# Performance work log

Measured on AMD Instinct MI355X. Metric: run time of the kernel, lower is better.

## Reference

```python
import jax, jax.numpy as jnp
import numpy as np

B, N, VF, EF, DV, DE, LN = 64, 64, 32, 16, 128, 128, 4
EPS_INNER = 128.0  # BatchNorm1d(MAX_N, internal_d_vert): 2nd positional arg is eps (faithful to source bug)
EPS_BN = 1e-5


def gev_layer(v_in, e_in, evW, evb, eW, eb, vW, vb, relu=True):
    act = jax.nn.relu if relu else (lambda x: x)
    ev = v_in @ evW + evb                                   # [B,N,De]
    # outer_v_sum: ev.unsqueeze(1) + ev.unsqueeze(2) -> [B,N,N,De]
    e_out = act(e_in @ eW + eb + ev[:, None, :, :] + ev[:, :, None, :])
    per_v_e = e_out.sum(axis=1)                             # sum-aggregate over dim 1
    v_out = act(jnp.concatenate([per_v_e, v_in], axis=-1) @ vW + vb)
    return v_out, e_out


def bn_flat(v, g, b):
    # BatchNorm1d(N*VF) on [B, N*VF] in training mode (biased var)
    x = v.reshape(-1, N * VF)
    mu = x.mean(axis=0)
    var = x.var(axis=0)
    x = (x - mu) * jax.lax.rsqrt(var + EPS_BN) * g + b
    return x.reshape(-1, N, VF)


def bn_inner(v, g, b):
    # BatchNorm1d(MAX_N, eps=128) on [B, N, D]: channels are the N axis, stats over (B, D)
    mu = v.mean(axis=(0, 2), keepdims=True)
    var = v.var(axis=(0, 2), keepdims=True)
    return (v - mu) * jax.lax.rsqrt(var + EPS_INNER) * g[None, :, None] + b[None, :, None]


def setup_inputs() -> dict:
    key = jax.random.key(0)
    ks = jax.random.split(key, 24)
    s = 0.01  # force_lin_init with init_noise=0.01, biases zero
    nrm = lambda k, shp: jax.random.normal(k, shp, dtype=jnp.float32) * s
    inp = {
        "v": jax.random.normal(ks[0], (B, N, VF), dtype=jnp.float32),
        "e": jax.random.normal(ks[1], (B, N, N, EF), dtype=jnp.float32),
        "bn_in_g": jnp.ones((N * VF,), jnp.float32),
        "bn_in_b": jnp.zeros((N * VF,), jnp.float32),
        "g1_evW": nrm(ks[2], (VF, DE)), "g1_evb": jnp.zeros((DE,), jnp.float32),
        "g1_eW": nrm(ks[3], (EF, DE)), "g1_eb": jnp.zeros((DE,), jnp.float32),
        "g1_vW": nrm(ks[4], (VF + DE, DV)), "g1_vb": jnp.zeros((DV,), jnp.float32),
        "inn_evW": nrm(ks[5], (LN, DV, DE)), "inn_evb": jnp.zeros((LN, DE), jnp.float32),
        "inn_eW": nrm(ks[6], (LN, DE, DE)), "inn_eb": jnp.zeros((LN, DE), jnp.float32),
        "inn_vW": nrm(ks[7], (LN, DV + DE, DV)), "inn_vb": jnp.zeros((LN, DV), jnp.float32),
        "bn_g": jnp.ones((LN, N), jnp.float32),
        "bn_b": jnp.zeros((LN, N), jnp.float32),
        "g3_evW": nrm(ks[8], (DV, 1)), "g3_evb": jnp.zeros((1,), jnp.float32),
        "g3_eW": nrm(ks[9], (DE, 1)), "g3_eb": jnp.zeros((1,), jnp.float32),
        "g3_vW": nrm(ks[10], (DV + 1, 1)), "g3_vb": jnp.zeros((1,), jnp.float32),
    }
    return inp


def reference(v, e, bn_in_g, bn_in_b, g1_evW, g1_evb, g1_eW, g1_eb, g1_vW, g1_vb,
              inn_evW, inn_evb, inn_eW, inn_eb, inn_vW, inn_vb, bn_g, bn_b,
              g3_evW, g3_evb, g3_eW, g3_eb, g3_vW, g3_vb):
    v = bn_flat(v, bn_in_g, bn_in_b)
    v, e = gev_layer(v, e, g1_evW, g1_evb, g1_eW, g1_eb, g1_vW, g1_vb)
    for i in range(LN):
        v_next, e_next = gev_layer(v, e, inn_evW[i], inn_evb[i], inn_eW[i], inn_eb[i], inn_vW[i], inn_vb[i])
        v = v_next + v  # resnet
        e = e_next + e
        v = bn_inner(v, bn_g[i], bn_b[i])
    v, e = gev_layer(v, e, g3_evW, g3_evb, g3_eW, g3_eb, g3_vW, g3_vb, relu=False)
    return v, e
```

## Files before the change

### kernel.cpp

```cpp
#include <hip/hip_runtime.h>
#include <hip/hip_bf16.h>


typedef __bf16 bf16_t;
typedef __bf16 bf16x8 __attribute__((ext_vector_type(8)));
typedef __bf16 bf16x4 __attribute__((ext_vector_type(4)));
typedef float f32x4 __attribute__((ext_vector_type(4)));

__device__ __forceinline__ void bar_lgkm() {
  asm volatile("s_waitcnt lgkmcnt(0)\n\ts_barrier" ::: "memory");
}

__global__ __launch_bounds__(256) void k_prep(const float* __restrict__ vin,
    const float* __restrict__ g, const float* __restrict__ bt,
    const float* __restrict__ eW, float* __restrict__ v0,
    bf16_t* __restrict__ Wt, float* __restrict__ stats) {
  const int blk = blockIdx.x, tid = threadIdx.x;
  if (blk < 8) {
    int ch = blk * 256 + tid;
    float s = 0.f, s2 = 0.f;
    for (int b = 0; b < 64; ++b) { float x = vin[b * 2048 + ch]; s += x; s2 += x * x; }
    float mu = s * (1.f / 64.f);
    float var = s2 * (1.f / 64.f) - mu * mu;
    float sc = rsqrtf(var + 1e-5f) * g[ch];
    float bb = bt[ch];
    for (int b = 0; b < 64; ++b) {
      float x = vin[b * 2048 + ch];
      v0[b * 2048 + ch] = (x - mu) * sc + bb;
    }
  } else if (blk < 264) {
    int idx = (blk - 8) * 256 + tid;
    int l = idx >> 14, r = idx & 16383, n = r >> 7, k = r & 127;
    Wt[idx] = (bf16_t)eW[(l << 14) + (k << 7) + n];
  } else {
    for (int i = tid; i < 512; i += 256) stats[i] = 0.f;
  }
}

template <int K>
__global__ __launch_bounds__(128) void k_ev(const float* __restrict__ v_in,
    const float* __restrict__ W, const float* __restrict__ bias,
    float* __restrict__ out) {
  __shared__ float rows[8][K];
  const int r0 = blockIdx.x * 8;
  const int c = threadIdx.x;
  for (int idx = c; idx < 8 * K; idx += 128) {
    int rr = idx / K, kk = idx % K;
    rows[rr][kk] = v_in[(r0 + rr) * K + kk];
  }
  __syncthreads();
  float acc[8];
  const float bv = bias[c];
#pragma unroll
  for (int r = 0; r < 8; ++r) acc[r] = bv;
  for (int k4 = 0; k4 < K; k4 += 4) {
    float w0 = W[(k4 + 0) * 128 + c], w1 = W[(k4 + 1) * 128 + c];
    float w2 = W[(k4 + 2) * 128 + c], w3 = W[(k4 + 3) * 128 + c];
#pragma unroll
    for (int r = 0; r < 8; ++r) {
      float4 x = *(const float4*)&rows[r][k4];
      acc[r] += x.x * w0 + x.y * w1 + x.z * w2 + x.w * w3;
    }
  }
#pragma unroll
  for (int r = 0; r < 8; ++r) out[(r0 + r) * 128 + c] = acc[r];
}

__global__ __launch_bounds__(128) void k_evbn(float* __restrict__ v,
    const float* __restrict__ stats, const float* __restrict__ g,
    const float* __restrict__ bt, const float* __restrict__ W,
    const float* __restrict__ bias, float* __restrict__ out) {
  __shared__ float rows[8][128];
  const int r0 = blockIdx.x * 8;
  const int c = threadIdx.x;
#pragma unroll
  for (int rr = 0; rr < 8; ++rr) {
    int n = (r0 + rr) & 63;
    float mu = stats[n] * (1.f / 8192.f);
    float var = stats[64 + n] * (1.f / 8192.f) - mu * mu;
    float sc = rsqrtf(var + 128.f) * g[n];
    float x = (v[(r0 + rr) * 128 + c] - mu) * sc + bt[n];
    rows[rr][c] = x;
    v[(r0 + rr) * 128 + c] = x;
  }
  __syncthreads();
  float acc[8];
  const float bv = bias[c];
#pragma unroll
  for (int r = 0; r < 8; ++r) acc[r] = bv;
  for (int k4 = 0; k4 < 128; k4 += 4) {
    float w0 = W[(k4 + 0) * 128 + c], w1 = W[(k4 + 1) * 128 + c];
    float w2 = W[(k4 + 2) * 128 + c], w3 = W[(k4 + 3) * 128 + c];
#pragma unroll
    for (int r = 0; r < 8; ++r) {
      float4 x = *(const float4*)&rows[r][k4];
      acc[r] += x.x * w0 + x.y * w1 + x.z * w2 + x.w * w3;
    }
  }
#pragma unroll
  for (int r = 0; r < 8; ++r) out[(r0 + r) * 128 + c] = acc[r];
}

__global__ __launch_bounds__(256) void k_edge_g1(const float* __restrict__ e0,
    const float* __restrict__ eW, const float* __restrict__ eb,
    const float* __restrict__ ev, bf16_t* __restrict__ e_ws,
    float* __restrict__ pve) {
  __shared__ bf16_t A0s[2][64][40];
  __shared__ bf16_t Os[2][64][136];
  const int b = blockIdx.x >> 5, j0 = (blockIdx.x & 31) * 2;
  const int tid = threadIdx.x;
  const int lane = tid & 63, w = tid >> 6;
  const int quad = lane >> 4, l16 = lane & 15;
#pragma unroll
  for (int t = 0; t < 2; ++t) {
    int idx = tid + t * 256;
    int row = idx >> 3, off = (idx & 7) * 4;
    int jc = off >> 4, k = off & 15;
    f32x4 x = *(const f32x4*)&e0[((b * 64 + row) * 64 + j0) * 16 + off];
    bf16x4 y;
#pragma unroll
    for (int r = 0; r < 4; ++r) y[r] = (bf16_t)x[r];
    *(bf16x4*)&A0s[jc][row][k] = y;
    bf16x4 z = {(bf16_t)0.f, (bf16_t)0.f, (bf16_t)0.f, (bf16_t)0.f};
    *(bf16x4*)&A0s[jc][row][16 + k] = z;
  }
  const int c0[2] = {w * 32 + quad * 4, w * 32 + 16 + quad * 4};
  bf16x8 wf[2];
#pragma unroll
  for (int nt = 0; nt < 2; ++nt) {
    const int c = w * 32 + nt * 16 + l16;
#pragma unroll
    for (int jj = 0; jj < 8; ++jj)
      wf[nt][jj] = (quad < 2) ? (bf16_t)eW[(quad * 8 + jj) * 128 + c] : (bf16_t)0.f;
  }
  f32x4 acc[2][4][2];
  {
    f32x4 ebv[2], evj[2][2], evi[4][2];
#pragma unroll
    for (int nt = 0; nt < 2; ++nt) {
      ebv[nt] = *(const f32x4*)&eb[c0[nt]];
#pragma unroll
      for (int jc = 0; jc < 2; ++jc)
        evj[jc][nt] = *(const f32x4*)&ev[(b * 64 + j0 + jc) * 128 + c0[nt]];
#pragma unroll
      for (int mt = 0; mt < 4; ++mt)
        evi[mt][nt] = *(const f32x4*)&ev[(b * 64 + mt * 16 + l16) * 128 + c0[nt]];
    }
#pragma unroll
    for (int jc = 0; jc < 2; ++jc)
#pragma unroll
      for (int mt = 0; mt < 4; ++mt)
#pragma unroll
        for (int nt = 0; nt < 2; ++nt)
          acc[jc][mt][nt] = ebv[nt] + evj[jc][nt] + evi[mt][nt];
  }
  __syncthreads();
#pragma unroll
  for (int jc = 0; jc < 2; ++jc) {
#pragma unroll
    for (int mt = 0; mt < 4; ++mt) {
      bf16x8 ef = *(const bf16x8*)&A0s[jc][mt * 16 + l16][quad * 8];
#pragma unroll
      for (int nt = 0; nt < 2; ++nt)
        acc[jc][mt][nt] = __builtin_amdgcn_mfma_f32_16x16x32_bf16(wf[nt], ef, acc[jc][mt][nt], 0, 0, 0);
    }
  }
#pragma unroll
  for (int jc = 0; jc < 2; ++jc) {
#pragma unroll
    for (int nt = 0; nt < 2; ++nt) {
      f32x4 ps = {0.f, 0.f, 0.f, 0.f};
#pragma unroll
      for (int mt = 0; mt < 4; ++mt) {
        const int i = mt * 16 + l16;
        bf16x4 outv;
#pragma unroll
        for (int r = 0; r < 4; ++r) {
          float vv = fmaxf(acc[jc][mt][nt][r], 0.f);
          ps[r] += vv;
          outv[r] = (bf16_t)vv;
        }
        *(bf16x4*)&Os[jc][i][c0[nt]] = outv;
      }
#pragma unroll
      for (int m = 1; m <= 8; m <<= 1) {
#pragma unroll
        for (int r = 0; r < 4; ++r) ps[r] += __shfl_xor(ps[r], m);
      }
      if (l16 == 0) *(f32x4*)&pve[(b * 64 + j0 + jc) * 128 + c0[nt]] = ps;
    }
  }
  __syncthreads();
#pragma unroll
  for (int t = 0; t < 8; ++t) {
    int idx = tid + t * 256;
    int row = idx >> 5, off = (idx & 31) * 8;
    int jc = off >> 7, c = off & 127;
    *(int4*)&e_ws[((b * 64 + row) * 64 + j0) * 128 + off] = *(const int4*)&Os[jc][row][c];
  }
}

__global__ __launch_bounds__(128) void k_vg1_ev(const float* __restrict__ pve,
    const float* __restrict__ v0, const float* __restrict__ vW,
    const float* __restrict__ vb, const float* __restrict__ evW,
    const float* __restrict__ evb, float* __restrict__ v, float* __restrict__ ev) {
  __shared__ float in[8][160];
  __shared__ float vr[8][128];
  const int r0 = blockIdx.x * 8;
  const int c = threadIdx.x;
#pragma unroll
  for (int t = 0; t < 8; ++t) {
    int idx = c + t * 128;
    int rr = idx >> 7, k = idx & 127;
    in[rr][k] = pve[(r0 + rr) * 128 + k];
  }
#pragma unroll
  for (int t = 0; t < 2; ++t) {
    int idx = c + t * 128;
    int rr = idx >> 5, k = idx & 31;
    in[rr][128 + k] = v0[(r0 + rr) * 32 + k];
  }
  __syncthreads();
  float acc[8];
  const float bv = vb[c];
#pragma unroll
  for (int r = 0; r < 8; ++r) acc[r] = bv;
  for (int k4 = 0; k4 < 160; k4 += 4) {
    float w0 = vW[(k4 + 0) * 128 + c], w1 = vW[(k4 + 1) * 128 + c];
    float w2 = vW[(k4 + 2) * 128 + c], w3 = vW[(k4 + 3) * 128 + c];
#pragma unroll
    for (int r = 0; r < 8; ++r) {
      float4 x = *(const float4*)&in[r][k4];
      acc[r] += x.x * w0 + x.y * w1 + x.z * w2 + x.w * w3;
    }
  }
#pragma unroll
  for (int r = 0; r < 8; ++r) {
    float val = fmaxf(acc[r], 0.f);
    vr[r][c] = val;
    v[(r0 + r) * 128 + c] = val;
  }
  __syncthreads();
  float acc2[8];
  const float bv2 = evb[c];
#pragma unroll
  for (int r = 0; r < 8; ++r) acc2[r] = bv2;
  for (int k4 = 0; k4 < 128; k4 += 4) {
    float w0 = evW[(k4 + 0) * 128 + c], w1 = evW[(k4 + 1) * 128 + c];
    float w2 = evW[(k4 + 2) * 128 + c], w3 = evW[(k4 + 3) * 128 + c];
#pragma unroll
    for (int r = 0; r < 8; ++r) {
      float4 x = *(const float4*)&vr[r][k4];
      acc2[r] += x.x * w0 + x.y * w1 + x.z * w2 + x.w * w3;
    }
  }
#pragma unroll
  for (int r = 0; r < 8; ++r) ev[(r0 + r) * 128 + c] = acc2[r];
}

template <bool LAST>
__global__ __launch_bounds__(256) void k_edge_inner(bf16_t* __restrict__ e_ws,
    const bf16_t* __restrict__ Wt, const float* __restrict__ eb,
    const float* __restrict__ ev, float* __restrict__ pve,
    const float* __restrict__ eW3, float* __restrict__ edt) {
  __shared__ bf16_t As[2][2][64][136];
  __shared__ float W3s[128];
  const int tid = threadIdx.x;
  const int lane = tid & 63, w = tid >> 6;
  const int quad = lane >> 4, l16 = lane & 15;
  const int b = blockIdx.x >> 4;
  const int jg = (blockIdx.x & 15) * 4;
  const int c0[2] = {w * 32 + quad * 4, w * 32 + 16 + quad * 4};
  bf16x8 wf[2][4];
#pragma unroll
  for (int nt = 0; nt < 2; ++nt)
#pragma unroll
    for (int ks = 0; ks < 4; ++ks)
      wf[nt][ks] = *(const bf16x8*)&Wt[(w * 32 + nt * 16 + l16) * 128 + ks * 32 + quad * 8];
  f32x4 ebv[2], evi[4][2];
#pragma unroll
  for (int nt = 0; nt < 2; ++nt) {
    ebv[nt] = *(const f32x4*)&eb[c0[nt]];
#pragma unroll
    for (int mt = 0; mt < 4; ++mt)
      evi[mt][nt] = *(const f32x4*)&ev[(b * 64 + mt * 16 + l16) * 128 + c0[nt]];
  }
  if (LAST) {
    if (tid < 128) W3s[tid] = eW3[tid];
  }
  int4 stg[8];
#pragma unroll
  for (int u = 0; u < 8; ++u) {
    int idx = tid + u * 256;
    stg[u] = *(const int4*)&e_ws[((b * 64 + (idx >> 5)) * 64 + jg) * 128 + (idx & 31) * 8];
  }
  f32x4 evj[2][2];
#pragma unroll
  for (int jc = 0; jc < 2; ++jc)
#pragma unroll
    for (int nt = 0; nt < 2; ++nt)
      evj[jc][nt] = *(const f32x4*)&ev[(b * 64 + jg + jc) * 128 + c0[nt]];
#pragma unroll
  for (int u = 0; u < 8; ++u) {
    int idx = tid + u * 256;
    int off = (idx & 31) * 8;
    *(int4*)&As[0][off >> 7][idx >> 5][off & 127] = stg[u];
  }
  bar_lgkm();
#pragma unroll
  for (int p = 0; p < 2; ++p) {
    const int j0 = jg + p * 2;
    int4 stg2[8];
    f32x4 evj2[2][2];
    if (p == 0) {
#pragma unroll
      for (int u = 0; u < 8; ++u) {
        int idx = tid + u * 256;
        stg2[u] = *(const int4*)&e_ws[((b * 64 + (idx >> 5)) * 64 + jg + 2) * 128 + (idx & 31) * 8];
      }
#pragma unroll
      for (int jc = 0; jc < 2; ++jc)
#pragma unroll
        for (int nt = 0; nt < 2; ++nt)
          evj2[jc][nt] = *(const f32x4*)&ev[(b * 64 + jg + 2 + jc) * 128 + c0[nt]];
    }
    f32x4 acc[2][4][2];
#pragma unroll
    for (int jc = 0; jc < 2; ++jc)
#pragma unroll
      for (int mt = 0; mt < 4; ++mt)
#pragma unroll
        for (int nt = 0; nt < 2; ++nt)
          acc[jc][mt][nt] = ebv[nt] + evj[jc][nt] + evi[mt][nt];
#pragma unroll
    for (int ks = 0; ks < 4; ++ks) {
      bf16x8 ef[2][4];
#pragma unroll
      for (int jc = 0; jc < 2; ++jc)
#pragma unroll
        for (int mt = 0; mt < 4; ++mt)
          ef[jc][mt] = *(const bf16x8*)&As[p][jc][mt * 16 + l16][ks * 32 + quad * 8];
#pragma unroll
      for (int jc = 0; jc < 2; ++jc)
#pragma unroll
        for (int mt = 0; mt < 4; ++mt)
#pragma unroll
          for (int nt = 0; nt < 2; ++nt)
            acc[jc][mt][nt] = __builtin_amdgcn_mfma_f32_16x16x32_bf16(wf[nt][ks], ef[jc][mt], acc[jc][mt][nt], 0, 0, 0);
    }
    bar_lgkm();
#pragma unroll
    for (int jc = 0; jc < 2; ++jc) {
#pragma unroll
      for (int nt = 0; nt < 2; ++nt) {
        f32x4 ps = {0.f, 0.f, 0.f, 0.f};
#pragma unroll
        for (int mt = 0; mt < 4; ++mt) {
          const int i = mt * 16 + l16;
          bf16x4 eo = *(const bf16x4*)&As[p][jc][i][c0[nt]];
          bf16x4 outv;
#pragma unroll
          for (int r = 0; r < 4; ++r) {
            float vv = fmaxf(acc[jc][mt][nt][r], 0.f);
            ps[r] += vv;
            outv[r] = (bf16_t)(vv + (float)eo[r]);
          }
          *(bf16x4*)&As[p][jc][i][c0[nt]] = outv;
        }
#pragma unroll
        for (int m = 1; m <= 8; m <<= 1) {
#pragma unroll
          for (int r = 0; r < 4; ++r) ps[r] += __shfl_xor(ps[r], m);
        }
        if (l16 == 0) *(f32x4*)&pve[(b * 64 + j0 + jc) * 128 + c0[nt]] = ps;
      }
    }
    bar_lgkm();
    if (!LAST) {
#pragma unroll
      for (int u = 0; u < 8; ++u) {
        int idx = tid + u * 256;
        int off = (idx & 31) * 8;
        *(int4*)&e_ws[((b * 64 + (idx >> 5)) * 64 + j0) * 128 + off] =
            *(const int4*)&As[p][off >> 7][idx >> 5][off & 127];
      }
    } else {
      const int i = tid >> 2, q = tid & 3;
#pragma unroll
      for (int jc = 0; jc < 2; ++jc) {
        float d = 0.f;
#pragma unroll
        for (int u = 0; u < 32; ++u) d += (float)As[p][jc][i][q * 32 + u] * W3s[q * 32 + u];
        d += __shfl_xor(d, 1);
        d += __shfl_xor(d, 2);
        if (q == 0) edt[(b * 64 + j0 + jc) * 64 + i] = d;
      }
    }
    if (p == 0) {
#pragma unroll
      for (int u = 0; u < 8; ++u) {
        int idx = tid + u * 256;
        int off = (idx & 31) * 8;
        *(int4*)&As[1][off >> 7][idx >> 5][off & 127] = stg2[u];
      }
#pragma unroll
      for (int jc = 0; jc < 2; ++jc) {
        evj[jc][0] = evj2[jc][0];
        evj[jc][1] = evj2[jc][1];
      }
      bar_lgkm();
    }
  }
}

__global__ __launch_bounds__(128) void k_v_inner(const float* __restrict__ pve,
    float* __restrict__ v, const float* __restrict__ vW,
    const float* __restrict__ vb, float* __restrict__ stats) {
  __shared__ float in[8][256];
  __shared__ float outs[8][132];
  const int r0 = blockIdx.x * 8;
  const int c = threadIdx.x;
#pragma unroll
  for (int t = 0; t < 8; ++t) {
    int idx = c + t * 128;
    int rr = idx >> 7, k = idx & 127;
    in[rr][k] = pve[(r0 + rr) * 128 + k];
    in[rr][128 + k] = v[(r0 + rr) * 128 + k];
  }
  __syncthreads();
  float acc[8];
  const float bv = vb[c];
#pragma unroll
  for (int r = 0; r < 8; ++r) acc[r] = bv;
  for (int k4 = 0; k4 < 256; k4 += 4) {
    float w0 = vW[(k4 + 0) * 128 + c], w1 = vW[(k4 + 1) * 128 + c];
    float w2 = vW[(k4 + 2) * 128 + c], w3 = vW[(k4 + 3) * 128 + c];
#pragma unroll
    for (int r = 0; r < 8; ++r) {
      float4 x = *(const float4*)&in[r][k4];
      acc[r] += x.x * w0 + x.y * w1 + x.z * w2 + x.w * w3;
    }
  }
#pragma unroll
  for (int r = 0; r < 8; ++r) {
    float val = fmaxf(acc[r], 0.f) + in[r][128 + c];
    outs[r][c] = val;
    v[(r0 + r) * 128 + c] = val;
  }
  __syncthreads();
  if (c < 8) {
    float s = 0.f, s2 = 0.f;
    for (int k = 0; k < 128; ++k) { float x = outs[c][k]; s += x; s2 += x * x; }
    int n = (r0 + c) & 63;
    atomicAdd(&stats[n], s);
    atomicAdd(&stats[64 + n], s2);
  }
}

__global__ __launch_bounds__(256) void k_g3(const float* __restrict__ vv,
    const float* __restrict__ stats3, const float* __restrict__ g,
    const float* __restrict__ bt, const float* __restrict__ evW3,
    const float* __restrict__ evb3, const float* __restrict__ eb3,
    const float* __restrict__ edt, const float* __restrict__ vW3,
    const float* __restrict__ vb3, float* __restrict__ out_v,
    float* __restrict__ out_e) {
  __shared__ float vbn[64][132];
  __shared__ float edts[64][68];
  __shared__ float scs[64], shs[64];
  __shared__ float W3e[128];
  __shared__ float vWs[132];
  __shared__ float ev3s[64];
  __shared__ float pj[4][64];
  const int b = blockIdx.x, tid = threadIdx.x;
  if (tid < 64) {
    float mu = stats3[tid] * (1.f / 8192.f);
    float var = stats3[64 + tid] * (1.f / 8192.f) - mu * mu;
    float sc = rsqrtf(var + 128.f) * g[tid];
    scs[tid] = sc;
    shs[tid] = bt[tid] - mu * sc;
  }
  if (tid < 128) W3e[tid] = evW3[tid];
  if (tid < 129) vWs[tid] = vW3[tid];
  __syncthreads();
#pragma unroll
  for (int t = 0; t < 8; ++t) {
    int idx = t * 1024 + tid * 4;
    int row = idx >> 7, cc = idx & 127;
    f32x4 x = *(const f32x4*)&vv[(b * 64 + row) * 128 + cc];
    *(f32x4*)&vbn[row][cc] = x * scs[row] + shs[row];
  }
#pragma unroll
  for (int t = 0; t < 4; ++t) {
    int idx = t * 1024 + tid * 4;
    int j = idx >> 6, i = idx & 63;
    *(f32x4*)&edts[j][i] = *(const f32x4*)&edt[(b * 64 + j) * 64 + i];
  }
  __syncthreads();
  {
    int i = tid >> 2, q = tid & 3;
    float d = 0.f;
#pragma unroll
    for (int u = 0; u < 32; ++u) d += vbn[i][q * 32 + u] * W3e[q * 32 + u];
    d += __shfl_xor(d, 1);
    d += __shfl_xor(d, 2);
    if (q == 0) ev3s[i] = d + evb3[0];
  }
  __syncthreads();
  {
    int q = tid >> 6, j = tid & 63;
    float s = 0.f;
    const float e3 = eb3[0];
    const float evj = ev3s[j];
#pragma unroll
    for (int r = 0; r < 16; ++r) {
      int i = q * 16 + r;
      float val = edts[j][i] + e3 + ev3s[i] + evj;
      out_e[(b * 64 + i) * 64 + j] = val;
      s += val;
    }
    pj[q][j] = s;
  }
  __syncthreads();
  {
    int n = tid >> 2, q = tid & 3;
    float d = 0.f;
#pragma unroll
    for (int u = 0; u < 32; ++u) d += vbn[n][q * 32 + u] * vWs[1 + q * 32 + u];
    d += __shfl_xor(d, 1);
    d += __shfl_xor(d, 2);
    if (q == 0) {
      float p3 = pj[0][n] + pj[1][n] + pj[2][n] + pj[3][n];
      out_v[b * 64 + n] = d + p3 * vWs[0] + vb3[0];
    }
  }
}

extern "C" void kernel_launch(void* const* d_in, const int* in_sizes, int n_in,
                              void* d_out, int out_size, void* d_ws, size_t ws_size,
                              hipStream_t stream) {
  const float* in_v    = (const float*)d_in[0];
  const float* in_e    = (const float*)d_in[1];
  const float* bn_in_g = (const float*)d_in[2];
  const float* bn_in_b = (const float*)d_in[3];
  const float* g1_evW  = (const float*)d_in[4];
  const float* g1_evb  = (const float*)d_in[5];
  const float* g1_eW   = (const float*)d_in[6];
  const float* g1_eb   = (const float*)d_in[7];
  const float* g1_vW   = (const float*)d_in[8];
  const float* g1_vb   = (const float*)d_in[9];
  const float* inn_evW = (const float*)d_in[10];
  const float* inn_evb = (const float*)d_in[11];
  const float* inn_eW  = (const float*)d_in[12];
  const float* inn_eb  = (const float*)d_in[13];
  const float* inn_vW  = (const float*)d_in[14];
  const float* inn_vb  = (const float*)d_in[15];
  const float* bn_g    = (const float*)d_in[16];
  const float* bn_b    = (const float*)d_in[17];
  const float* g3_evW  = (const float*)d_in[18];
  const float* g3_evb  = (const float*)d_in[19];
  const float* g3_eW   = (const float*)d_in[20];
  const float* g3_eb   = (const float*)d_in[21];
  const float* g3_vW   = (const float*)d_in[22];
  const float* g3_vb   = (const float*)d_in[23];

  char* ws = (char*)d_ws;
  bf16_t* e_ws = (bf16_t*)(ws);
  float* v     = (float*)(ws + 67108864);
  float* ev    = (float*)(ws + 69206016);
  float* pve   = (float*)(ws + 71303168);
  float* v0    = (float*)(ws + 73400320);
  bf16_t* Wt   = (bf16_t*)(ws + 73924608);
  float* edt   = (float*)(ws + 74055680);
  float* stats = (float*)(ws + 75104256);

  float* out_v = (float*)d_out;
  float* out_e = (float*)d_out + 4096;

  k_prep<<<265, 256, 0, stream>>>(in_v, bn_in_g, bn_in_b, inn_eW, v0, Wt, stats);

  k_ev<32><<<512, 128, 0, stream>>>(v0, g1_evW, g1_evb, ev);
  k_edge_g1<<<2048, 256, 0, stream>>>(in_e, g1_eW, g1_eb, ev, e_ws, pve);
  k_vg1_ev<<<512, 128, 0, stream>>>(pve, v0, g1_vW, g1_vb, inn_evW, inn_evb, v, ev);

  for (int l = 0; l < 4; ++l) {
    if (l > 0)
      k_evbn<<<512, 128, 0, stream>>>(v, stats + (l - 1) * 128, bn_g + (l - 1) * 64,
                                      bn_b + (l - 1) * 64, inn_evW + l * 16384,
                                      inn_evb + l * 128, ev);
    if (l < 3)
      k_edge_inner<false><<<1024, 256, 0, stream>>>(e_ws, Wt + l * 16384,
          inn_eb + l * 128, ev, pve, g3_eW, edt);
    else
      k_edge_inner<true><<<1024, 256, 0, stream>>>(e_ws, Wt + l * 16384,
          inn_eb + l * 128, ev, pve, g3_eW, edt);
    k_v_inner<<<512, 128, 0, stream>>>(pve, v, inn_vW + l * 32768, inn_vb + l * 128,
                                       stats + l * 128);
  }

  k_g3<<<64, 256, 0, stream>>>(v, stats + 384, bn_g + 192, bn_b + 192,
                               g3_evW, g3_evb, g3_eb, edt, g3_vW, g3_vb,
                               out_v, out_e);
}
```

Baseline: 455.1 us.

## Double vertex-kernel thread counts and split edge kernel into single-tile blocks

New measurement: 368.8 us. -19.0%, faster.

```diff
diff --git a/kernel.cpp b/kernel.cpp
--- a/kernel.cpp
+++ b/kernel.cpp
@@ -38,67 +38,71 @@
 }
 
 template <int K>
-__global__ __launch_bounds__(128) void k_ev(const float* __restrict__ v_in,
+__global__ __launch_bounds__(256) void k_ev(const float* __restrict__ v_in,
     const float* __restrict__ W, const float* __restrict__ bias,
     float* __restrict__ out) {
-  __shared__ float rows[8][K];
+  __shared__ float rows_s[8][K];
   const int r0 = blockIdx.x * 8;
-  const int c = threadIdx.x;
-  for (int idx = c; idx < 8 * K; idx += 128) {
+  const int tid = threadIdx.x;
+  const int c = tid & 127, h = tid >> 7;
+  for (int idx = tid; idx < 8 * K; idx += 256) {
     int rr = idx / K, kk = idx % K;
-    rows[rr][kk] = v_in[(r0 + rr) * K + kk];
-  }
-  __syncthreads();
-  float acc[8];
+    rows_s[rr][kk] = v_in[(r0 + rr) * K + kk];
+  }
+  __syncthreads();
+  float acc[4];
   const float bv = bias[c];
 #pragma unroll
-  for (int r = 0; r < 8; ++r) acc[r] = bv;
+  for (int r = 0; r < 4; ++r) acc[r] = bv;
   for (int k4 = 0; k4 < K; k4 += 4) {
     float w0 = W[(k4 + 0) * 128 + c], w1 = W[(k4 + 1) * 128 + c];
     float w2 = W[(k4 + 2) * 128 + c], w3 = W[(k4 + 3) * 128 + c];
 #pragma unroll
-    for (int r = 0; r < 8; ++r) {
-      float4 x = *(const float4*)&rows[r][k4];
+    for (int r = 0; r < 4; ++r) {
+      float4 x = *(const float4*)&rows_s[h * 4 + r][k4];
       acc[r] += x.x * w0 + x.y * w1 + x.z * w2 + x.w * w3;
     }
   }
 #pragma unroll
-  for (int r = 0; r < 8; ++r) out[(r0 + r) * 128 + c] = acc[r];
-}
-
-__global__ __launch_bounds__(128) void k_evbn(float* __restrict__ v,
+  for (int r = 0; r < 4; ++r) out[(r0 + h * 4 + r) * 128 + c] = acc[r];
+}
+
+__global__ __launch_bounds__(256) void k_evbn(float* __restrict__ v,
     const float* __restrict__ stats, const float* __restrict__ g,
     const float* __restrict__ bt, const float* __restrict__ W,
     const float* __restrict__ bias, float* __restrict__ out) {
-  __shared__ float rows[8][128];
+  __shared__ float rows_s[8][128];
   const int r0 = blockIdx.x * 8;
-  const int c = threadIdx.x;
-#pragma unroll
-  for (int rr = 0; rr < 8; ++rr) {
+  const int tid = threadIdx.x;
+  const int c = tid & 127, h = tid >> 7;
+#pragma unroll
+  for (int u = 0; u < 4; ++u) {
+    int idx = u * 256 + tid;
+    int rr = idx >> 7, k = idx & 127;
     int n = (r0 + rr) & 63;
     float mu = stats[n] * (1.f / 8192.f);
     float var = stats[64 + n] * (1.f / 8192.f) - mu * mu;
     float sc = rsqrtf(var + 128.f) * g[n];
-    float x = (v[(r0 + rr) * 128 + c] - mu) * sc + bt[n];
-    rows[rr][c] = x;
-    v[(r0 + rr) * 128 + c] = x;
-  }
-  __syncthreads();
-  float acc[8];
+    float x = (v[(r0 + rr) * 128 + k] - mu) * sc + bt[n];
+    rows_s[rr][k] = x;
+    v[(r0 + rr) * 128 + k] = x;
+  }
+  __syncthreads();
+  float acc[4];
   const float bv = bias[c];
 #pragma unroll
-  for (int r = 0; r < 8; ++r) acc[r] = bv;
+  for (int r = 0; r < 4; ++r) acc[r] = bv;
   for (int k4 = 0; k4 < 128; k4 += 4) {
     float w0 = W[(k4 + 0) * 128 + c], w1 = W[(k4 + 1) * 128 + c];
     float w2 = W[(k4 + 2) * 128 + c], w3 = W[(k4 + 3) * 128 + c];
 #pragma unroll
-    for (int r = 0; r < 8; ++r) {
-      float4 x = *(const float4*)&rows[r][k4];
+    for (int r = 0; r < 4; ++r) {
+      float4 x = *(const float4*)&rows_s[h * 4 + r][k4];
       acc[r] += x.x * w0 + x.y * w1 + x.z * w2 + x.w * w3;
     }
   }
 #pragma unroll
-  for (int r = 0; r < 8; ++r) out[(r0 + r) * 128 + c] = acc[r];
+  for (int r = 0; r < 4; ++r) out[(r0 + h * 4 + r) * 128 + c] = acc[r];
 }
 
 __global__ __launch_bounds__(256) void k_edge_g1(const float* __restrict__ e0,
@@ -200,62 +204,61 @@
   }
 }
 
-__global__ __launch_bounds__(128) void k_vg1_ev(const float* __restrict__ pve,
+__global__ __launch_bounds__(256) void k_vg1_ev(const float* __restrict__ pve,
     const float* __restrict__ v0, const float* __restrict__ vW,
     const float* __restrict__ vb, const float* __restrict__ evW,
     const float* __restrict__ evb, float* __restrict__ v, float* __restrict__ ev) {
-  __shared__ float in[8][160];
+  __shared__ float in_s[8][160];
   __shared__ float vr[8][128];
   const int r0 = blockIdx.x * 8;
-  const int c = threadIdx.x;
-#pragma unroll
-  for (int t = 0; t < 8; ++t) {
-    int idx = c + t * 128;
+  const int tid = threadIdx.x;
+  const int c = tid & 127, h = tid >> 7;
+#pragma unroll
+  for (int u = 0; u < 4; ++u) {
+    int idx = u * 256 + tid;
     int rr = idx >> 7, k = idx & 127;
-    in[rr][k] = pve[(r0 + rr) * 128 + k];
-  }
-#pragma unroll
-  for (int t = 0; t < 2; ++t) {
-    int idx = c + t * 128;
-    int rr = idx >> 5, k = idx & 31;
-    in[rr][128 + k] = v0[(r0 + rr) * 32 + k];
-  }
-  __syncthreads();
-  float acc[8];
+    in_s[rr][k] = pve[(r0 + rr) * 128 + k];
+  }
+  {
+    int rr = tid >> 5, k = tid & 31;
+    in_s[rr][128 + k] = v0[(r0 + rr) * 32 + k];
+  }
+  __syncthreads();
+  float acc[4];
   const float bv = vb[c];
 #pragma unroll
-  for (int r = 0; r < 8; ++r) acc[r] = bv;
+  for (int r = 0; r < 4; ++r) acc[r] = bv;
   for (int k4 = 0; k4 < 160; k4 += 4) {
     float w0 = vW[(k4 + 0) * 128 + c], w1 = vW[(k4 + 1) * 128 + c];
     float w2 = vW[(k4 + 2) * 128 + c], w3 = vW[(k4 + 3) * 128 + c];
 #pragma unroll
-    for (int r = 0; r < 8; ++r) {
-      float4 x = *(const float4*)&in[r][k4];
+    for (int r = 0; r < 4; ++r) {
+      float4 x = *(const float4*)&in_s[h * 4 + r][k4];
       acc[r] += x.x * w0 + x.y * w1 + x.z * w2 + x.w * w3;
     }
   }
 #pragma unroll
-  for (int r = 0; r < 8; ++r) {
+  for (int r = 0; r < 4; ++r) {
     float val = fmaxf(acc[r], 0.f);
-    vr[r][c] = val;
-    v[(r0 + r) * 128 + c] = val;
-  }
-  __syncthreads();
-  float acc2[8];
+    vr[h * 4 + r][c] = val;
+    v[(r0 + h * 4 + r) * 128 + c] = val;
+  }
+  __syncthreads();
+  float acc2[4];
   const float bv2 = evb[c];
 #pragma unroll
-  for (int r = 0; r < 8; ++r) acc2[r] = bv2;
+  for (int r = 0; r < 4; ++r) acc2[r] = bv2;
   for (int k4 = 0; k4 < 128; k4 += 4) {
     float w0 = evW[(k4 + 0) * 128 + c], w1 = evW[(k4 + 1) * 128 + c];
     float w2 = evW[(k4 + 2) * 128 + c], w3 = evW[(k4 + 3) * 128 + c];
 #pragma unroll
-    for (int r = 0; r < 8; ++r) {
-      float4 x = *(const float4*)&vr[r][k4];
+    for (int r = 0; r < 4; ++r) {
+      float4 x = *(const float4*)&vr[h * 4 + r][k4];
       acc2[r] += x.x * w0 + x.y * w1 + x.z * w2 + x.w * w3;
     }
   }
 #pragma unroll
-  for (int r = 0; r < 8; ++r) ev[(r0 + r) * 128 + c] = acc2[r];
+  for (int r = 0; r < 4; ++r) ev[(r0 + h * 4 + r) * 128 + c] = acc2[r];
 }
 
 template <bool LAST>
@@ -263,68 +266,42 @@
     const bf16_t* __restrict__ Wt, const float* __restrict__ eb,
     const float* __restrict__ ev, float* __restrict__ pve,
     const float* __restrict__ eW3, float* __restrict__ edt) {
-  __shared__ bf16_t As[2][2][64][136];
+  __shared__ bf16_t As[2][64][136];
   __shared__ float W3s[128];
+  const int b = blockIdx.x >> 5, j0 = (blockIdx.x & 31) * 2;
   const int tid = threadIdx.x;
   const int lane = tid & 63, w = tid >> 6;
   const int quad = lane >> 4, l16 = lane & 15;
-  const int b = blockIdx.x >> 4;
-  const int jg = (blockIdx.x & 15) * 4;
-  const int c0[2] = {w * 32 + quad * 4, w * 32 + 16 + quad * 4};
+  int4 stg[8];
+#pragma unroll
+  for (int t = 0; t < 8; ++t) {
+    int idx = tid + t * 256;
+    int row = idx >> 5, off = (idx & 31) * 8;
+    stg[t] = *(const int4*)&e_ws[((b * 64 + row) * 64 + j0) * 128 + off];
+  }
+  if (LAST) {
+    if (tid < 128) W3s[tid] = eW3[tid];
+  }
   bf16x8 wf[2][4];
 #pragma unroll
   for (int nt = 0; nt < 2; ++nt)
 #pragma unroll
     for (int ks = 0; ks < 4; ++ks)
       wf[nt][ks] = *(const bf16x8*)&Wt[(w * 32 + nt * 16 + l16) * 128 + ks * 32 + quad * 8];
-  f32x4 ebv[2], evi[4][2];
-#pragma unroll
-  for (int nt = 0; nt < 2; ++nt) {
-    ebv[nt] = *(const f32x4*)&eb[c0[nt]];
-#pragma unroll
-    for (int mt = 0; mt < 4; ++mt)
-      evi[mt][nt] = *(const f32x4*)&ev[(b * 64 + mt * 16 + l16) * 128 + c0[nt]];
-  }
-  if (LAST) {
-    if (tid < 128) W3s[tid] = eW3[tid];
-  }
-  int4 stg[8];
-#pragma unroll
-  for (int u = 0; u < 8; ++u) {
-    int idx = tid + u * 256;
-    stg[u] = *(const int4*)&e_ws[((b * 64 + (idx >> 5)) * 64 + jg) * 128 + (idx & 31) * 8];
-  }
-  f32x4 evj[2][2];
-#pragma unroll
-  for (int jc = 0; jc < 2; ++jc)
-#pragma unroll
-    for (int nt = 0; nt < 2; ++nt)
-      evj[jc][nt] = *(const f32x4*)&ev[(b * 64 + jg + jc) * 128 + c0[nt]];
-#pragma unroll
-  for (int u = 0; u < 8; ++u) {
-    int idx = tid + u * 256;
-    int off = (idx & 31) * 8;
-    *(int4*)&As[0][off >> 7][idx >> 5][off & 127] = stg[u];
-  }
-  bar_lgkm();
-#pragma unroll
-  for (int p = 0; p < 2; ++p) {
-    const int j0 = jg + p * 2;
-    int4 stg2[8];
-    f32x4 evj2[2][2];
-    if (p == 0) {
-#pragma unroll
-      for (int u = 0; u < 8; ++u) {
-        int idx = tid + u * 256;
-        stg2[u] = *(const int4*)&e_ws[((b * 64 + (idx >> 5)) * 64 + jg + 2) * 128 + (idx & 31) * 8];
-      }
+  const int c0[2] = {w * 32 + quad * 4, w * 32 + 16 + quad * 4};
+  f32x4 acc[2][4][2];
+  {
+    f32x4 ebv[2], evj[2][2], evi[4][2];
+#pragma unroll
+    for (int nt = 0; nt < 2; ++nt) {
+      ebv[nt] = *(const f32x4*)&eb[c0[nt]];
 #pragma unroll
       for (int jc = 0; jc < 2; ++jc)
-#pragma unroll
-        for (int nt = 0; nt < 2; ++nt)
-          evj2[jc][nt] = *(const f32x4*)&ev[(b * 64 + jg + 2 + jc) * 128 + c0[nt]];
-    }
-    f32x4 acc[2][4][2];
+        evj[jc][nt] = *(const f32x4*)&ev[(b * 64 + j0 + jc) * 128 + c0[nt]];
+#pragma unroll
+      for (int mt = 0; mt < 4; ++mt)
+        evi[mt][nt] = *(const f32x4*)&ev[(b * 64 + mt * 16 + l16) * 128 + c0[nt]];
+    }
 #pragma unroll
     for (int jc = 0; jc < 2; ++jc)
 #pragma unroll
@@ -332,128 +309,136 @@
 #pragma unroll
         for (int nt = 0; nt < 2; ++nt)
           acc[jc][mt][nt] = ebv[nt] + evj[jc][nt] + evi[mt][nt];
-#pragma unroll
-    for (int ks = 0; ks < 4; ++ks) {
-      bf16x8 ef[2][4];
-#pragma unroll
-      for (int jc = 0; jc < 2; ++jc)
-#pragma unroll
-        for (int mt = 0; mt < 4; ++mt)
-          ef[jc][mt] = *(const bf16x8*)&As[p][jc][mt * 16 + l16][ks * 32 + quad * 8];
-#pragma unroll
-      for (int jc = 0; jc < 2; ++jc)
-#pragma unroll
-        for (int mt = 0; mt < 4; ++mt)
-#pragma unroll
-          for (int nt = 0; nt < 2; ++nt)
-            acc[jc][mt][nt] = __builtin_amdgcn_mfma_f32_16x16x32_bf16(wf[nt][ks], ef[jc][mt], acc[jc][mt][nt], 0, 0, 0);
-    }
-    bar_lgkm();
+  }
+#pragma unroll
+  for (int t = 0; t < 8; ++t) {
+    int idx = tid + t * 256;
+    int row = idx >> 5, off = (idx & 31) * 8;
+    *(int4*)&As[off >> 7][row][off & 127] = stg[t];
+  }
+  bar_lgkm();
+#pragma unroll
+  for (int ks = 0; ks < 4; ++ks) {
+    bf16x8 ef[2][4];
+#pragma unroll
+    for (int jc = 0; jc < 2; ++jc)
+#pragma unroll
+      for (int mt = 0; mt < 4; ++mt)
+        ef[jc][mt] = *(const bf16x8*)&As[jc][mt * 16 + l16][ks * 32 + quad * 8];
+#pragma unroll
+    for (int jc = 0; jc < 2; ++jc)
+#pragma unroll
+      for (int mt = 0; mt < 4; ++mt)
+#pragma unroll
+        for (int nt = 0; nt < 2; ++nt)
+          acc[jc][mt][nt] = __builtin_amdgcn_mfma_f32_16x16x32_bf16(wf[nt][ks], ef[jc][mt], acc[jc][mt][nt], 0, 0, 0);
+  }
+  bar_lgkm();
+#pragma unroll
+  for (int jc = 0; jc < 2; ++jc) {
+#pragma unroll
+    for (int nt = 0; nt < 2; ++nt) {
+      f32x4 ps = {0.f, 0.f, 0.f, 0.f};
+#pragma unroll
+      for (int mt = 0; mt < 4; ++mt) {
+        const int i = mt * 16 + l16;
+        bf16x4 eo = *(const bf16x4*)&As[jc][i][c0[nt]];
+        bf16x4 outv;
+#pragma unroll
+        for (int r = 0; r < 4; ++r) {
+          float vv = fmaxf(acc[jc][mt][nt][r], 0.f);
+          ps[r] += vv;
+          outv[r] = (bf16_t)(vv + (float)eo[r]);
+        }
+        *(bf16x4*)&As[jc][i][c0[nt]] = outv;
+      }
+#pragma unroll
+      for (int m = 1; m <= 8; m <<= 1) {
+#pragma unroll
+        for (int r = 0; r < 4; ++r) ps[r] += __shfl_xor(ps[r], m);
+      }
+      if (l16 == 0) *(f32x4*)&pve[(b * 64 + j0 + jc) * 128 + c0[nt]] = ps;
+    }
+  }
+  bar_lgkm();
+  if (!LAST) {
+#pragma unroll
+    for (int t = 0; t < 8; ++t) {
+      int idx = tid + t * 256;
+      int row = idx >> 5, off = (idx & 31) * 8;
+      *(int4*)&e_ws[((b * 64 + row) * 64 + j0) * 128 + off] =
+          *(const int4*)&As[off >> 7][row][off & 127];
+    }
+  } else {
+    const int i = tid >> 2, q = tid & 3;
 #pragma unroll
     for (int jc = 0; jc < 2; ++jc) {
-#pragma unroll
-      for (int nt = 0; nt < 2; ++nt) {
-        f32x4 ps = {0.f, 0.f, 0.f, 0.f};
-#pragma unroll
-        for (int mt = 0; mt < 4; ++mt) {
-          const int i = mt * 16 + l16;
-          bf16x4 eo = *(const bf16x4*)&As[p][jc][i][c0[nt]];
-          bf16x4 outv;
-#pragma unroll
-          for (int r = 0; r < 4; ++r) {
-            float vv = fmaxf(acc[jc][mt][nt][r], 0.f);
-            ps[r] += vv;
-            outv[r] = (bf16_t)(vv + (float)eo[r]);
-          }
-          *(bf16x4*)&As[p][jc][i][c0[nt]] = outv;
-        }
-#pragma unroll
-        for (int m = 1; m <= 8; m <<= 1) {
-#pragma unroll
-          for (int r = 0; r < 4; ++r) ps[r] += __shfl_xor(ps[r], m);
-        }
-        if (l16 == 0) *(f32x4*)&pve[(b * 64 + j0 + jc) * 128 + c0[nt]] = ps;
+      float d = 0.f;
+#pragma unroll
+      for (int t = 0; t < 4; ++t) {
+        bf16x8 x = *(const bf16x8*)&As[jc][i][q * 32 + t * 8];
+#pragma unroll
+        for (int u = 0; u < 8; ++u) d += (float)x[u] * W3s[q * 32 + t * 8 + u];
       }
-    }
-    bar_lgkm();
-    if (!LAST) {
-#pragma unroll
-      for (int u = 0; u < 8; ++u) {
-        int idx = tid + u * 256;
-        int off = (idx & 31) * 8;
-        *(int4*)&e_ws[((b * 64 + (idx >> 5)) * 64 + j0) * 128 + off] =
-            *(const int4*)&As[p][off >> 7][idx >> 5][off & 127];
-      }
-    } else {
-      const int i = tid >> 2, q = tid & 3;
-#pragma unroll
-      for (int jc = 0; jc < 2; ++jc) {
-        float d = 0.f;
-#pragma unroll
-        for (int u = 0; u < 32; ++u) d += (float)As[p][jc][i][q * 32 + u] * W3s[q * 32 + u];
-        d += __shfl_xor(d, 1);
-        d += __shfl_xor(d, 2);
-        if (q == 0) edt[(b * 64 + j0 + jc) * 64 + i] = d;
-      }
-    }
-    if (p == 0) {
-#pragma unroll
-      for (int u = 0; u < 8; ++u) {
-        int idx = tid + u * 256;
-        int off = (idx & 31) * 8;
-        *(int4*)&As[1][off >> 7][idx >> 5][off & 127] = stg2[u];
-      }
-#pragma unroll
-      for (int jc = 0; jc < 2; ++jc) {
-        evj[jc][0] = evj2[jc][0];
-        evj[jc][1] = evj2[jc][1];
-      }
-      bar_lgkm();
-    }
-  }
-}
-
-__global__ __launch_bounds__(128) void k_v_inner(const float* __restrict__ pve,
+      d += __shfl_xor(d, 1);
+      d += __shfl_xor(d, 2);
+      if (q == 0) edt[(b * 64 + j0 + jc) * 64 + i] = d;
+    }
+  }
+}
+
+__global__ __launch_bounds__(256) void k_v_inner(const float* __restrict__ pve,
     float* __restrict__ v, const float* __restrict__ vW,
     const float* __restrict__ vb, float* __restrict__ stats) {
-  __shared__ float in[8][256];
+  __shared__ float in_s[8][256];
   __shared__ float outs[8][132];
+  __shared__ float part[16][2];
   const int r0 = blockIdx.x * 8;
-  const int c = threadIdx.x;
-#pragma unroll
-  for (int t = 0; t < 8; ++t) {
-    int idx = c + t * 128;
+  const int tid = threadIdx.x;
+  const int c = tid & 127, h = tid >> 7;
+#pragma unroll
+  for (int u = 0; u < 4; ++u) {
+    int idx = u * 256 + tid;
     int rr = idx >> 7, k = idx & 127;
-    in[rr][k] = pve[(r0 + rr) * 128 + k];
-    in[rr][128 + k] = v[(r0 + rr) * 128 + k];
-  }
-  __syncthreads();
-  float acc[8];
+    in_s[rr][k] = pve[(r0 + rr) * 128 + k];
+    in_s[rr][128 + k] = v[(r0 + rr) * 128 + k];
+  }
+  __syncthreads();
+  float acc[4];
   const float bv = vb[c];
 #pragma unroll
-  for (int r = 0; r < 8; ++r) acc[r] = bv;
+  for (int r = 0; r < 4; ++r) acc[r] = bv;
   for (int k4 = 0; k4 < 256; k4 += 4) {
     float w0 = vW[(k4 + 0) * 128 + c], w1 = vW[(k4 + 1) * 128 + c];
     float w2 = vW[(k4 + 2) * 128 + c], w3 = vW[(k4 + 3) * 128 + c];
 #pragma unroll
-    for (int r = 0; r < 8; ++r) {
-      float4 x = *(const float4*)&in[r][k4];
+    for (int r = 0; r < 4; ++r) {
+      float4 x = *(const float4*)&in_s[h * 4 + r][k4];
       acc[r] += x.x * w0 + x.y * w1 + x.z * w2 + x.w * w3;
     }
   }
 #pragma unroll
-  for (int r = 0; r < 8; ++r) {
-    float val = fmaxf(acc[r], 0.f) + in[r][128 + c];
-    outs[r][c] = val;
-    v[(r0 + r) * 128 + c] = val;
-  }
-  __syncthreads();
-  if (c < 8) {
+  for (int r = 0; r < 4; ++r) {
+    float val = fmaxf(acc[r], 0.f) + in_s[h * 4 + r][128 + c];
+    outs[h * 4 + r][c] = val;
+    v[(r0 + h * 4 + r) * 128 + c] = val;
+  }
+  __syncthreads();
+  if (tid < 16) {
+    int rr = tid >> 1, half = tid & 1;
     float s = 0.f, s2 = 0.f;
-    for (int k = 0; k < 128; ++k) { float x = outs[c][k]; s += x; s2 += x * x; }
-    int n = (r0 + c) & 63;
-    atomicAdd(&stats[n], s);
-    atomicAdd(&stats[64 + n], s2);
+    for (int k = 0; k < 64; ++k) {
+      float x = outs[rr][half * 64 + k];
+      s += x; s2 += x * x;
+    }
+    part[tid][0] = s;
+    part[tid][1] = s2;
+  }
+  __syncthreads();
+  if (tid < 8) {
+    int n = (r0 + tid) & 63;
+    atomicAdd(&stats[n], part[tid * 2][0] + part[tid * 2 + 1][0]);
+    atomicAdd(&stats[64 + n], part[tid * 2][1] + part[tid * 2 + 1][1]);
   }
 }
 
@@ -578,22 +563,22 @@
 
   k_prep<<<265, 256, 0, stream>>>(in_v, bn_in_g, bn_in_b, inn_eW, v0, Wt, stats);
 
-  k_ev<32><<<512, 128, 0, stream>>>(v0, g1_evW, g1_evb, ev);
+  k_ev<32><<<512, 256, 0, stream>>>(v0, g1_evW, g1_evb, ev);
   k_edge_g1<<<2048, 256, 0, stream>>>(in_e, g1_eW, g1_eb, ev, e_ws, pve);
-  k_vg1_ev<<<512, 128, 0, stream>>>(pve, v0, g1_vW, g1_vb, inn_evW, inn_evb, v, ev);
+  k_vg1_ev<<<512, 256, 0, stream>>>(pve, v0, g1_vW, g1_vb, inn_evW, inn_evb, v, ev);
 
   for (int l = 0; l < 4; ++l) {
     if (l > 0)
-      k_evbn<<<512, 128, 0, stream>>>(v, stats + (l - 1) * 128, bn_g + (l - 1) * 64,
+      k_evbn<<<512, 256, 0, stream>>>(v, stats + (l - 1) * 128, bn_g + (l - 1) * 64,
                                       bn_b + (l - 1) * 64, inn_evW + l * 16384,
                                       inn_evb + l * 128, ev);
     if (l < 3)
-      k_edge_inner<false><<<1024, 256, 0, stream>>>(e_ws, Wt + l * 16384,
+      k_edge_inner<false><<<2048, 256, 0, stream>>>(e_ws, Wt + l * 16384,
           inn_eb + l * 128, ev, pve, g3_eW, edt);
     else
-      k_edge_inner<true><<<1024, 256, 0, stream>>>(e_ws, Wt + l * 16384,
+      k_edge_inner<true><<<2048, 256, 0, stream>>>(e_ws, Wt + l * 16384,
           inn_eb + l * 128, ev, pve, g3_eW, edt);
-    k_v_inner<<<512, 128, 0, stream>>>(pve, v, inn_vW + l * 32768, inn_vb + l * 128,
+    k_v_inner<<<512, 256, 0, stream>>>(pve, v, inn_vW + l * 32768, inn_vb + l * 128,
                                        stats + l * 128);
   }
 
```
